# Performance work log

Measured on AMD Instinct MI355X. Metric: run time of the kernel, lower is better.

The kernel has to match this reference:

```python
import jax, jax.numpy as jnp
import numpy as np

N_BUS, N_LINE, N_GEN, N_LOAD = 1000, 2000, 100, 500
MAXSTEPS = 10  # matches ACOPF.maxsteps default
RIDGE = 1e-6  # tiny Tikhonov term for a robust normal-equation solve


def setup_inputs() -> dict:
    rng = np.random.default_rng(0)
    perm = rng.permutation(N_BUS)
    gen_buses = np.sort(perm[:N_GEN]).astype(np.int32)
    load_buses = np.sort(perm[N_GEN:N_GEN + N_LOAD]).astype(np.int32)
    ref_bus_idx = int(gen_buses[0])  # slack bus is a generator bus
    nongen_idx = np.setdiff1d(np.arange(N_BUS), gen_buses).astype(np.int32)
    nonref_idx = np.delete(np.arange(N_BUS), ref_bus_idx).astype(np.int32)
    line_from = rng.integers(0, N_BUS, N_LINE).astype(np.int32)
    line_to = ((line_from + rng.integers(1, N_BUS, N_LINE)) % N_BUS).astype(np.int32)

    ks = jax.random.split(jax.random.key(0), 12)
    u = lambda k, n, lo, hi: jax.random.uniform(k, (n,), jnp.float32, lo, hi)
    line_g = u(ks[0], N_LINE, 1.0, 5.0)
    line_b = -u(ks[1], N_LINE, 5.0, 15.0)
    shunt_g = u(ks[2], N_BUS, 0.0, 0.05)
    shunt_b = u(ks[3], N_BUS, 0.0, 0.05)
    tap = 1.0 + u(ks[4], N_LINE, -0.05, 0.05)
    shift = u(ks[5], N_LINE, -0.05, 0.05)
    charging = u(ks[6], N_LINE, 0.0, 0.05)
    P_gen = u(ks[7], N_GEN, 0.0, 0.5)
    V_gen = jnp.ones((N_GEN,), jnp.float32)
    P_load = u(ks[8], N_LOAD, 0.0, 0.1)
    Q_load = u(ks[9], N_LOAD, 0.0, 0.05)
    bus_v_limits = jnp.stack(
        [jnp.full((N_BUS,), 0.94, jnp.float32), jnp.full((N_BUS,), 1.06, jnp.float32)], axis=1)

    return dict(
        line_g=line_g, line_b=line_b, shunt_g=shunt_g, shunt_b=shunt_b,
        tap=tap, shift=shift, charging=charging,
        P_gen=P_gen, V_gen=V_gen, P_load=P_load, Q_load=Q_load,
        bus_v_limits=bus_v_limits,
        line_from=jnp.asarray(line_from), line_to=jnp.asarray(line_to),
        gen_buses=jnp.asarray(gen_buses), load_buses=jnp.asarray(load_buses),
        nongen_idx=jnp.asarray(nongen_idx), nonref_idx=jnp.asarray(nonref_idx),
        ref_bus_idx=ref_bus_idx,
    )


def _admittance_coo(line_from, line_to, line_g, line_b, shunt_g, shunt_b, tap, shift, charging, n_bus):
    # Standard pi-model branch admittances with transformer taps/phase shifts.
    ys = line_g.astype(jnp.complex64) + 1j * line_b.astype(jnp.complex64)
    bc = 1j * (charging.astype(jnp.complex64) / 2)
    tc = tap.astype(jnp.complex64) * jnp.exp(1j * shift.astype(jnp.complex64))
    Yff = (ys + bc) / (tap * tap)
    Ytt = ys + bc
    Yft = -ys / jnp.conj(tc)
    Ytf = -ys / tc
    diag = jnp.arange(n_bus, dtype=line_from.dtype)
    rows = jnp.concatenate([line_from, line_to, line_from, line_to, diag])
    cols = jnp.concatenate([line_from, line_to, line_to, line_from, diag])
    vals = jnp.concatenate([Yff, Ytt, Yft, Ytf,
                            shunt_g.astype(jnp.complex64) + 1j * shunt_b.astype(jnp.complex64)])
    return rows, cols, vals


def reference(line_g, line_b, shunt_g, shunt_b, tap, shift, charging,
              P_gen, V_gen, P_load, Q_load, bus_v_limits,
              line_from, line_to, gen_buses, load_buses,
              nongen_idx, nonref_idx, ref_bus_idx):
    n_bus = shunt_g.shape[0]
    n_nongen = nongen_idx.shape[0]
    rows, cols, vals = _admittance_coo(line_from, line_to, line_g, line_b,
                                       shunt_g, shunt_b, tap, shift, charging, n_bus)

    def injections(Vm, Va):
        V = Vm * jnp.exp(1j * Va)  # [n_bus] complex64
        current = jax.ops.segment_sum(vals * V[cols], rows, num_segments=n_bus)  # sparse Y @ V
        S = V * jnp.conj(current)
        return S.real, S.imag

    def residual(x):
        Vm = jnp.zeros(n_bus, jnp.float32).at[gen_buses].set(V_gen).at[nongen_idx].set(x[:n_nongen])
        Va = jnp.zeros(n_bus, jnp.float32).at[nonref_idx].set(x[n_nongen:])
        P, Q = injections(Vm, Va)
        P = P.at[gen_buses].add(-P_gen).at[load_buses].add(-P_load)
        Q = Q.at[load_buses].add(-Q_load)
        return jnp.concatenate([P[nonref_idx], Q[nongen_idx]])

    @jax.checkpoint
    def gn_step(x):
        r = residual(x)
        J = jax.jacfwd(residual)(x)  # [n_res, n_x]
        JtJ = J.T @ J + RIDGE * jnp.eye(J.shape[1], dtype=J.dtype)
        dx = jnp.linalg.solve(JtJ, J.T @ r)
        return x - dx

    x = jnp.concatenate([jnp.ones(n_nongen, jnp.float32),
                         jnp.zeros(n_bus - 1, jnp.float32)])
    for _ in range(MAXSTEPS):
        x = gn_step(x)

    r_final = residual(x)
    acopf_residual = (r_final ** 2).sum()

    Vm = jnp.zeros(n_bus, jnp.float32).at[gen_buses].set(V_gen).at[nongen_idx].set(x[:n_nongen])
    Va = jnp.zeros(n_bus, jnp.float32).at[nonref_idx].set(x[n_nongen:])

    # complete_powers
    P, Q = injections(Vm, Va)
    P = P.at[gen_buses].add(-P_gen).at[load_buses].add(-P_load)
    Q = Q.at[load_buses].add(-Q_load)
    Q_gen = Q[gen_buses]
    P_ref = P[ref_bus_idx]
    Q_ref = Q[ref_bus_idx]

    # voltage constraint violations
    V_min, V_max = bus_v_limits[:, 0], bus_v_limits[:, 1]
    V_violation = jax.nn.relu(Vm - V_max) + jax.nn.relu(V_min - Vm)

    return Vm, Va, Q_gen, P_ref, Q_ref, acopf_residual, V_violation
```

## Files before the change

### kernel.cpp

```cpp
#include <hip/hip_runtime.h>
#include <hip/hip_bf16.h>


#define NBUS 1000
#define NLINE 2000
#define NE   (2*NLINE)
#define NGEN 100
#define NLOAD 500
#define NTH 1024
#define NWAVE (NTH/64)
#define MAXSTEPS 10
#define KCG_MAX 600
#define RIDGE_F 1e-6f
#define TOL_REL 1e-10

struct Ws {
  int   vm_pos[NBUS];
  int   va_pos[NBUS];
  float Pspec[NBUS];
  float Qspec[NBUS];
  float Vgb[NBUS];
  int   rank_f[NLINE];
  int   rank_t[NLINE];
};

__device__ __forceinline__ float rdf(const void* p, int i, int bf) {
  if (bf) {
    unsigned int u = ((unsigned int)(((const unsigned short*)p)[i])) << 16;
    return __uint_as_float(u);
  }
  return ((const float*)p)[i];
}
__device__ __forceinline__ void wrf(void* p, int i, float v, int bf) {
  if (bf) {
    unsigned int u = __float_as_uint(v);
    unsigned int r = (u + 0x7fffu + ((u >> 16) & 1u)) >> 16;
    ((unsigned short*)p)[i] = (unsigned short)r;
  } else {
    ((float*)p)[i] = v;
  }
}
__device__ __forceinline__ int detect_bf(const void* p) {
  const unsigned short* h = (const unsigned short*)p;
  int ok = 1;
#pragma unroll
  for (int i = 0; i < 8; ++i) {
    float v = __uint_as_float(((unsigned int)h[i]) << 16);
    ok &= (v > 0.25f && v < 8.0f) ? 1 : 0;
  }
  return ok;
}
__device__ __forceinline__ int lbound(const int* a, int n, int v) {
  int lo = 0, hi = n;
  while (lo < hi) { int m = (lo + hi) >> 1; if (a[m] < v) lo = m + 1; else hi = m; }
  return lo;
}

struct In {
  const void *lg, *lb, *tp, *sh, *ch;
  const int *lf, *lt;
  int bf;
};
struct LineY { int f, t; float ffr, ffi, ttr, tti, ftr, fti, tfr, tfi; };

__device__ __forceinline__ LineY line_y(const In& I, int l) {
  LineY L;
  double g = rdf(I.lg, l, I.bf), b = rdf(I.lb, l, I.bf);
  double t = rdf(I.tp, l, I.bf), s = rdf(I.sh, l, I.bf);
  double c = rdf(I.ch, l, I.bf) * 0.5;
  double sn, cs;
  sincos(s, &sn, &cs);
  double it = 1.0 / t, it2 = it * it;
  L.f = I.lf[l]; L.t = I.lt[l];
  L.ffr = (float)(g * it2);                 L.ffi = (float)((b + c) * it2);
  L.ttr = (float)g;                         L.tti = (float)(b + c);
  L.ftr = (float)(-(g * cs - b * sn) * it); L.fti = (float)(-(g * sn + b * cs) * it);
  L.tfr = (float)(-(g * cs + b * sn) * it); L.tfi = (float)(-(b * cs - g * sn) * it);
  return L;
}

__device__ __forceinline__ float blk_sumf(float v, float* red) {
#pragma unroll
  for (int o = 32; o > 0; o >>= 1) v += __shfl_down(v, o, 64);
  if ((threadIdx.x & 63) == 0) red[threadIdx.x >> 6] = v;
  __syncthreads();
  const float4* r4 = (const float4*)red;
  float s = 0.f;
#pragma unroll
  for (int w = 0; w < NWAVE / 4; ++w) {
    float4 t = r4[w];
    s += t.x; s += t.y; s += t.z; s += t.w;
  }
  return s;
}

__global__ void setup_k(const void* lg, const void* Pg, const void* Vg,
                        const void* Pl, const void* Ql,
                        const int* gen_b, const int* load_b, const int* refp,
                        const int* lf, const int* lt,
                        Ws* __restrict__ W) {
  __shared__ int slf[NLINE], slt[NLINE];
  int bf = detect_bf(lg);
  int t = blockIdx.x * blockDim.x + threadIdx.x;
  for (int i = threadIdx.x; i < NLINE; i += blockDim.x) { slf[i] = lf[i]; slt[i] = lt[i]; }
  __syncthreads();
  int ref = refp[0];
  if (t < NBUS) {
    int gl = lbound(gen_b, NGEN, t);
    int isg = (gl < NGEN && gen_b[gl] == t) ? 1 : 0;
    int ll = lbound(load_b, NLOAD, t);
    int isl = (ll < NLOAD && load_b[ll] == t) ? 1 : 0;
    W->vm_pos[t] = isg ? -1 : (t - gl);
    W->va_pos[t] = (t == ref) ? -1 : (t - ((t > ref) ? 1 : 0));
    float ps = 0.f, qs = 0.f;
    if (isg) ps += rdf(Pg, gl, bf);
    if (isl) { ps += rdf(Pl, ll, bf); qs += rdf(Ql, ll, bf); }
    W->Pspec[t] = ps;
    W->Qspec[t] = qs;
    W->Vgb[t] = isg ? rdf(Vg, gl, bf) : 1.0f;
  }
  if (t < NLINE) {
    int f = slf[t], tt = slt[t], rf = 0, rt = 0;
    for (int l = 0; l < t; ++l) {
      int a = slf[l], b = slt[l];
      rf += (a == f) + (b == f);
      rt += (a == tt) + (b == tt);
    }
    W->rank_f[t] = rf;
    W->rank_t[t] = rt;
  }
}

__global__ void __launch_bounds__(NTH)
solver_k(const void* lg, const void* lb, const void* shg, const void* shb,
         const void* tp, const void* sh, const void* ch, const void* limits,
         const int* lf, const int* lt, const int* gen_b, const int* refp,
         const Ws* __restrict__ W, void* __restrict__ out) {
  __shared__ int rs_[NBUS + 1];
  __shared__ unsigned short cidx_[NE];
  __shared__ float2 fwd_[NE];
  __shared__ float2 rev_[NE];
  __shared__ float2 ev_[NE];
  __shared__ float2 stp_[NBUS];
  __shared__ float2 sts_[NBUS];
  __shared__ float2 ab_[NBUS];
  __shared__ float2 mk_[NBUS];
  __shared__ __align__(16) float red_[2][NWAVE];

  const int tid = threadIdx.x;
  const bool own = (tid < NBUS);
  In I;
  I.lg = lg; I.lb = lb; I.tp = tp; I.sh = sh; I.ch = ch;
  I.lf = lf; I.lt = lt;
  I.bf = detect_bf(lg);
  const int bf = I.bf;

  int* scanA = (int*)ev_;
  int* scanB = ((int*)ev_) + NTH;

  int vp = -1, ap = -1;
  float mng = 0.f, mnr = 0.f, Pspec = 0.f, Qspec = 0.f, Vgb = 1.f;
  if (own) {
    vp = W->vm_pos[tid]; ap = W->va_pos[tid];
    mng = (vp >= 0) ? 1.f : 0.f;
    mnr = (ap >= 0) ? 1.f : 0.f;
    Pspec = W->Pspec[tid]; Qspec = W->Qspec[tid]; Vgb = W->Vgb[tid];
    mk_[tid] = make_float2(mnr, mng);
  }
  scanA[tid] = 0;
  __syncthreads();
  for (int l = tid; l < NLINE; l += NTH) {
    atomicAdd(&scanA[lf[l]], 1);
    atomicAdd(&scanA[lt[l]], 1);
  }
  __syncthreads();
  {
    int* src = scanA; int* dst = scanB;
    for (int off = 1; off < NTH; off <<= 1) {
      int v = src[tid] + ((tid >= off) ? src[tid - off] : 0);
      dst[tid] = v;
      __syncthreads();
      int* t = src; src = dst; dst = t;
    }
    if (tid == 0) rs_[0] = 0;
    if (own) rs_[tid + 1] = src[tid];
  }
  __syncthreads();
  for (int l = tid; l < NLINE; l += NTH) {
    LineY L = line_y(I, l);
    int pf = rs_[L.f] + W->rank_f[l];
    int pt = rs_[L.t] + W->rank_t[l];
    cidx_[pf] = (unsigned short)L.t;
    fwd_[pf] = make_float2(L.ftr, L.fti);
    rev_[pf] = make_float2(L.tfr, L.tfi);
    ev_[pf]  = make_float2(L.ffr, L.ffi);
    cidx_[pt] = (unsigned short)L.f;
    fwd_[pt] = make_float2(L.tfr, L.tfi);
    rev_[pt] = make_float2(L.ftr, L.fti);
    ev_[pt]  = make_float2(L.ttr, L.tti);
  }
  __syncthreads();
  float Gkk = 0.f, Bkk = 0.f;
  int rs0 = 0, rs1 = 0;
  if (own) {
    rs0 = rs_[tid]; rs1 = rs_[tid + 1];
    double G = rdf(shg, tid, bf), B = rdf(shb, tid, bf);
    for (int e = rs0; e < rs1; ++e) { float2 d = ev_[e]; G += d.x; B += d.y; }
    Gkk = (float)G; Bkk = (float)B;
  }
  __syncthreads();

  #define EDGE_JVP_S(SRC) \
    for (int k = 0; k < 4; ++k) { \
      int e = tid + k * NTH; \
      if (e < NE) { \
        int j = cidx_[e]; float2 f = fwd_[e], v = SRC[j]; \
        ev_[e] = make_float2(f.x * v.x - f.y * v.y, f.x * v.y + f.y * v.x); \
      } \
    }
  #define EDGE_VJP(SRC) \
    for (int k = 0; k < 4; ++k) { \
      int e = tid + k * NTH; \
      if (e < NE) { \
        int j = cidx_[e]; float2 r = rev_[e], w = SRC[j]; \
        ev_[e] = make_float2(r.x * w.x + r.y * w.y, r.x * w.y - r.y * w.x); \
      } \
    }

  double xvm = 1.0, xva = 0.0;
  int par = 0;
  double gabs = 0.0;

  for (int outer = 0; outer < MAXSTEPS; ++outer) {
    float av = 0.f, bv = 0.f, ca = 1.f, sa = 0.f;
    if (own) {
      double Vm = (vp >= 0) ? xvm : (double)Vgb;
      double Va = (ap >= 0) ? xva : 0.0;
      double snd, csd;
      sincos(Va, &snd, &csd);
      ca = (float)csd; sa = (float)snd;
      av = (float)(Vm * csd); bv = (float)(Vm * snd);
      ab_[tid] = make_float2(av, bv);
    }
    __syncthreads();
    EDGE_JVP_S(ab_)
    __syncthreads();
    float cI = 0.f, dI = 0.f, wPp = 0.f, wQq = 0.f;
    float M11 = 0.f, M12 = 0.f, M22 = 0.f;
    if (own) {
      double cId = (double)Gkk * av - (double)Bkk * bv;
      double dId = (double)Gkk * bv + (double)Bkk * av;
      for (int e = rs0; e < rs1; ++e) { float2 v = ev_[e]; cId += v.x; dId += v.y; }
      cI = (float)cId; dI = (float)dId;
      double P = (double)av * cId + (double)bv * dId - (double)Pspec;
      double Q = (double)bv * cId - (double)av * dId - (double)Qspec;
      wPp = (float)(mnr * P); wQq = (float)(mng * Q);
      sts_[tid] = make_float2(wPp * av + wQq * bv, wPp * bv - wQq * av);
      float w1r = ca * cI + sa * dI, w1i = sa * cI - ca * dI;
      float mr = Gkk * ca - Bkk * sa, mi = -(Gkk * sa + Bkk * ca);
      float ur0 = av * mr - bv * mi, ui0 = av * mi + bv * mr;
      float Tr = w1r + ur0, Ti = w1i + ui0;
      float w2r = av * dI - bv * cI, w2i = av * cI + bv * dI;
      float wr0 = Gkk * av - Bkk * bv, wi0 = Gkk * bv + Bkk * av;
      float zr0 = av * wr0 + bv * wi0, zi0 = bv * wr0 - av * wi0;
      float Uor = w2r + zi0, Uoi = w2i - zr0;
      float Avv = mnr * Tr * Tr + mng * Ti * Ti;
      float Aaa = mnr * Uor * Uor + mng * Uoi * Uoi;
      float Ava = mnr * Tr * Uor + mng * Ti * Uoi;
      for (int e = rs0; e < rs1; ++e) {
        int j = cidx_[e]; float2 r = rev_[e], vj = ab_[j], mj = mk_[j];
        float mrr = r.x * ca - r.y * sa, mii = -(r.x * sa + r.y * ca);
        float ur = vj.x * mrr - vj.y * mii, ui = vj.x * mii + vj.y * mrr;
        float wr = r.x * av - r.y * bv, wi = r.x * bv + r.y * av;
        float zr = vj.x * wr + vj.y * wi, zi = vj.y * wr - vj.x * wi;
        Avv += mj.x * ur * ur + mj.y * ui * ui;
        Aaa += mj.x * zi * zi + mj.y * zr * zr;
        Ava += mj.x * ur * zi - mj.y * ui * zr;
      }
      float A11 = Avv + RIDGE_F, A22 = Aaa + RIDGE_F;
      if (vp >= 0 && ap >= 0) {
        float id = 1.f / (A11 * A22 - Ava * Ava);
        M11 = A22 * id; M22 = A11 * id; M12 = -Ava * id;
      } else if (vp >= 0) M11 = 1.f / A11;
      else if (ap >= 0)  M22 = 1.f / A22;
    }
    __syncthreads();
    EDGE_VJP(sts_)
    __syncthreads();
    float g0vm = 0.f, g0va = 0.f;
    if (own) {
      float cb = wPp * av + wQq * bv, db2 = wPp * bv - wQq * av;
      double sda = (double)wPp * cI - (double)wQq * dI + (double)Gkk * cb + (double)Bkk * db2;
      double sdb = (double)wPp * dI + (double)wQq * cI - (double)Bkk * cb + (double)Gkk * db2;
      for (int e = rs0; e < rs1; ++e) { float2 v = ev_[e]; sda += v.x; sdb += v.y; }
      g0vm = (float)(mng * (ca * sda + sa * sdb));
      g0va = (float)(mnr * (-bv * sda + av * sdb));
    }
    float rvm = g0vm, rva = g0va, dxvm = 0.f, dxva = 0.f;
    float zvm = M11 * rvm + M12 * rva, zva = M12 * rvm + M22 * rva;
    float pvm = zvm, pva = zva;
    float tzx = 0.f, tzy = 0.f, tpx = 0.f, tpy = 0.f;
    if (own) {
      tzx = zvm * ca - zva * bv; tzy = zvm * sa + zva * av;
      tpx = tzx; tpy = tzy;
      stp_[tid] = make_float2(tpx, tpy);
    }
    float part = own ? (rvm * zvm + rva * zva) : 0.f;
    double gamma = (double)blk_sumf(part, red_[par]); par ^= 1;
    const double gamma0 = gamma;
    if (outer == 0) gabs = 0.1 * TOL_REL * gamma0;
    const double thr = fmax(gamma0 * TOL_REL, gabs);

    if (gamma0 > thr) {
      for (int it = 0; it < KCG_MAX; ++it) {
        EDGE_JVP_S(stp_)
        __syncthreads();
        float qP = 0.f, qQ = 0.f;
        float dpart = 0.f;
        if (own) {
          float dc = Gkk * tpx - Bkk * tpy, dd = Gkk * tpy + Bkk * tpx;
          for (int e = rs0; e < rs1; ++e) { float2 v = ev_[e]; dc += v.x; dd += v.y; }
          float dP = tpx * cI + av * dc + tpy * dI + bv * dd;
          float dQ = tpy * cI + bv * dc - tpx * dI - av * dd;
          qP = mnr * dP; qQ = mng * dQ;
          sts_[tid] = make_float2(qP * av + qQ * bv, qP * bv - qQ * av);
          dpart = qP * dP + qQ * dQ + RIDGE_F * (pvm * pvm + pva * pva);
        }
        double delta = (double)blk_sumf(dpart, red_[par]); par ^= 1;
        if (!(delta > 0.0)) break;
        float af = (float)(gamma / delta);
        EDGE_VJP(sts_)
        __syncthreads();
        if (own) {
          dxvm += af * pvm; dxva += af * pva;
          float cb = qP * av + qQ * bv, db2 = qP * bv - qQ * av;
          float sda = qP * cI - qQ * dI + Gkk * cb + Bkk * db2;
          float sdb = qP * dI + qQ * cI - Bkk * cb + Gkk * db2;
          for (int e = rs0; e < rs1; ++e) { float2 v = ev_[e]; sda += v.x; sdb += v.y; }
          float yvm = mng * (ca * sda + sa * sdb);
          float yva = mnr * (-bv * sda + av * sdb);
          rvm -= af * (yvm + RIDGE_F * pvm);
          rva -= af * (yva + RIDGE_F * pva);
        }
        if ((it & 63) == 63) {
          float tda = 0.f, tdb = 0.f;
          if (own) {
            tda = dxvm * ca - dxva * bv;
            tdb = dxvm * sa + dxva * av;
            sts_[tid] = make_float2(tda, tdb);
          }
          __syncthreads();
          EDGE_JVP_S(sts_)
          __syncthreads();
          float rqP = 0.f, rqQ = 0.f;
          if (own) {
            float dc = Gkk * tda - Bkk * tdb, dd = Gkk * tdb + Bkk * tda;
            for (int e = rs0; e < rs1; ++e) { float2 v = ev_[e]; dc += v.x; dd += v.y; }
            float dP = tda * cI + av * dc + tdb * dI + bv * dd;
            float dQ = tdb * cI + bv * dc - tda * dI - av * dd;
            rqP = mnr * dP; rqQ = mng * dQ;
            sts_[tid] = make_float2(rqP * av + rqQ * bv, rqP * bv - rqQ * av);
          }
          __syncthreads();
          EDGE_VJP(sts_)
          __syncthreads();
          if (own) {
            float cb = rqP * av + rqQ * bv, db2 = rqP * bv - rqQ * av;
            float sda = rqP * cI - rqQ * dI + Gkk * cb + Bkk * db2;
            float sdb = rqP * dI + rqQ * cI - Bkk * cb + Gkk * db2;
            for (int e = rs0; e < rs1; ++e) { float2 v = ev_[e]; sda += v.x; sdb += v.y; }
            float tvm = mng * (ca * sda + sa * sdb);
            float tva = mnr * (-bv * sda + av * sdb);
            rvm = g0vm - tvm - RIDGE_F * dxvm;
            rva = g0va - tva - RIDGE_F * dxva;
          }
        }
        float gpart = 0.f;
        if (own) {
          zvm = M11 * rvm + M12 * rva; zva = M12 * rvm + M22 * rva;
          tzx = zvm * ca - zva * bv; tzy = zvm * sa + zva * av;
          gpart = rvm * zvm + rva * zva;
        }
        double gamma2 = (double)blk_sumf(gpart, red_[par]); par ^= 1;
        if (gamma2 <= thr || !(gamma2 > 0.0)) break;
        float bt = (float)(gamma2 / gamma);
        gamma = gamma2;
        if (own) {
          pvm = zvm + bt * pvm; pva = zva + bt * pva;
          tpx = tzx + bt * tpx; tpy = tzy + bt * tpy;
          stp_[tid] = make_float2(tpx, tpy);
        }
        __syncthreads();
      }
    }
    if (own) { xvm -= (double)dxvm; xva -= (double)dxva; }
    __syncthreads();
  }

  float Vmf = 1.f, Vaf = 0.f, av = 0.f, bv = 0.f;
  if (own) {
    double Vm = (vp >= 0) ? xvm : (double)Vgb;
    double Va = (ap >= 0) ? xva : 0.0;
    double snd, csd;
    sincos(Va, &snd, &csd);
    Vmf = (float)Vm; Vaf = (float)Va;
    av = (float)(Vm * csd); bv = (float)(Vm * snd);
    ab_[tid] = make_float2(av, bv);
  }
  __syncthreads();
  EDGE_JVP_S(ab_)
  __syncthreads();
  float P = 0.f, Q = 0.f;
  if (own) {
    double cId = (double)Gkk * av - (double)Bkk * bv;
    double dId = (double)Gkk * bv + (double)Bkk * av;
    for (int e = rs0; e < rs1; ++e) { float2 v = ev_[e]; cId += v.x; dId += v.y; }
    P = (float)((double)av * cId + (double)bv * dId - (double)Pspec);
    Q = (float)((double)bv * cId - (double)av * dId - (double)Qspec);
    sts_[tid] = make_float2(P, Q);
  }
  __syncthreads();
  float rpart = own ? (mnr * P * P + mng * Q * Q) : 0.f;
  float rsum = blk_sumf(rpart, red_[par]); par ^= 1;
  if (own) {
    wrf(out, tid, Vmf, bf);
    wrf(out, NBUS + tid, Vaf, bf);
    float vmin = rdf(limits, 2 * tid, bf), vmax = rdf(limits, 2 * tid + 1, bf);
    float viol = fmaxf(Vmf - vmax, 0.f) + fmaxf(vmin - Vmf, 0.f);
    wrf(out, 2103 + tid, viol, bf);
  }
  if (tid < NGEN) wrf(out, 2000 + tid, sts_[gen_b[tid]].y, bf);
  if (tid == 0) {
    int ref = refp[0];
    wrf(out, 2100, sts_[ref].x, bf);
    wrf(out, 2101, sts_[ref].y, bf);
    wrf(out, 2102, rsum, bf);
  }
}

extern "C" void kernel_launch(void* const* d_in, const int* in_sizes, int n_in,
                              void* d_out, int out_size, void* d_ws, size_t ws_size,
                              hipStream_t stream) {
  const void* line_g   = d_in[0];
  const void* line_b   = d_in[1];
  const void* shunt_g  = d_in[2];
  const void* shunt_b  = d_in[3];
  const void* tap      = d_in[4];
  const void* shift    = d_in[5];
  const void* charging = d_in[6];
  const void* P_gen    = d_in[7];
  const void* V_gen    = d_in[8];
  const void* P_load   = d_in[9];
  const void* Q_load   = d_in[10];
  const void* limits   = d_in[11];
  const int* line_from = (const int*)d_in[12];
  const int* line_to   = (const int*)d_in[13];
  const int* gen_b     = (const int*)d_in[14];
  const int* load_b    = (const int*)d_in[15];
  const int* refp      = (const int*)d_in[18];

  if (ws_size < sizeof(Ws)) return;
  Ws* W = (Ws*)d_ws;

  setup_k<<<dim3(8), dim3(256), 0, stream>>>(line_g, P_gen, V_gen, P_load, Q_load,
                                             gen_b, load_b, refp,
                                             line_from, line_to, W);
  solver_k<<<dim3(1), dim3(NTH), 0, stream>>>(line_g, line_b, shunt_g, shunt_b,
                                              tap, shift, charging, limits,
                                              line_from, line_to, gen_b, refp,
                                              W, d_out);
}
```

Baseline: 1.908 ms.

## Assign edges per wavefront to drop block barriers after edge products

```diff
diff --git a/kernel.cpp b/kernel.cpp
--- a/kernel.cpp
+++ b/kernel.cpp
@@ -140,7 +140,7 @@
   __shared__ unsigned short cidx_[NE];
   __shared__ float2 fwd_[NE];
   __shared__ float2 rev_[NE];
-  __shared__ float2 ev_[NE];
+  __shared__ float2 ev_[NE + NBUS];
   __shared__ float2 stp_[NBUS];
   __shared__ float2 sts_[NBUS];
   __shared__ float2 ab_[NBUS];
@@ -210,22 +210,43 @@
   }
   __syncthreads();
 
-  #define EDGE_JVP_S(SRC) \
-    for (int k = 0; k < 4; ++k) { \
-      int e = tid + k * NTH; \
-      if (e < NE) { \
-        int j = cidx_[e]; float2 f = fwd_[e], v = SRC[j]; \
-        ev_[e] = make_float2(f.x * v.x - f.y * v.y, f.x * v.y + f.y * v.x); \
+  const int prs0 = rs0 + tid, prs1 = rs1 + tid;
+
+  const int wv = tid >> 6, ln = tid & 63;
+  const int wb0 = wv * 64;
+  const int wb1 = (wb0 + 64 < NBUS) ? wb0 + 64 : NBUS;
+  const int ws0 = rs_[wb0], ws1 = rs_[wb1];
+  int   sj[8]; float2 sf[8], sr[8]; int sp[8]; bool sv[8];
+#pragma unroll
+  for (int k = 0; k < 8; ++k) {
+    int s = ws0 + ln + 64 * k;
+    bool v = (s < ws1);
+    sv[k] = v;
+    int ss = v ? s : ws0;
+    sj[k] = cidx_[ss]; sf[k] = fwd_[ss]; sr[k] = rev_[ss];
+    int lo = wb0, hi = wb1;
+    while (lo + 1 < hi) { int m = (lo + hi) >> 1; if (rs_[m] <= ss) lo = m; else hi = m; }
+    sp[k] = ss + lo;
+  }
+
+  #define WJVP(SRC) \
+    _Pragma("unroll") \
+    for (int k = 0; k < 8; ++k) { \
+      if (sv[k]) { \
+        int j = sj[k]; float2 f = sf[k], v = SRC[j]; \
+        ev_[sp[k]] = make_float2(f.x * v.x - f.y * v.y, f.x * v.y + f.y * v.x); \
       } \
-    }
-  #define EDGE_VJP(SRC) \
-    for (int k = 0; k < 4; ++k) { \
-      int e = tid + k * NTH; \
-      if (e < NE) { \
-        int j = cidx_[e]; float2 r = rev_[e], w = SRC[j]; \
-        ev_[e] = make_float2(r.x * w.x + r.y * w.y, r.x * w.y - r.y * w.x); \
+    } \
+    asm volatile("" ::: "memory");
+  #define WVJP(SRC) \
+    _Pragma("unroll") \
+    for (int k = 0; k < 8; ++k) { \
+      if (sv[k]) { \
+        int j = sj[k]; float2 r = sr[k], w = SRC[j]; \
+        ev_[sp[k]] = make_float2(r.x * w.x + r.y * w.y, r.x * w.y - r.y * w.x); \
       } \
-    }
+    } \
+    asm volatile("" ::: "memory");
 
   double xvm = 1.0, xva = 0.0;
   int par = 0;
@@ -243,14 +264,13 @@
       ab_[tid] = make_float2(av, bv);
     }
     __syncthreads();
-    EDGE_JVP_S(ab_)
-    __syncthreads();
+    WJVP(ab_)
     float cI = 0.f, dI = 0.f, wPp = 0.f, wQq = 0.f;
     float M11 = 0.f, M12 = 0.f, M22 = 0.f;
     if (own) {
       double cId = (double)Gkk * av - (double)Bkk * bv;
       double dId = (double)Gkk * bv + (double)Bkk * av;
-      for (int e = rs0; e < rs1; ++e) { float2 v = ev_[e]; cId += v.x; dId += v.y; }
+      for (int e = prs0; e < prs1; ++e) { float2 v = ev_[e]; cId += v.x; dId += v.y; }
       cI = (float)cId; dI = (float)dId;
       double P = (double)av * cId + (double)bv * dId - (double)Pspec;
       double Q = (double)bv * cId - (double)av * dId - (double)Qspec;
@@ -285,14 +305,13 @@
       else if (ap >= 0)  M22 = 1.f / A22;
     }
     __syncthreads();
-    EDGE_VJP(sts_)
-    __syncthreads();
+    WVJP(sts_)
     float g0vm = 0.f, g0va = 0.f;
     if (own) {
       float cb = wPp * av + wQq * bv, db2 = wPp * bv - wQq * av;
       double sda = (double)wPp * cI - (double)wQq * dI + (double)Gkk * cb + (double)Bkk * db2;
       double sdb = (double)wPp * dI + (double)wQq * cI - (double)Bkk * cb + (double)Gkk * db2;
-      for (int e = rs0; e < rs1; ++e) { float2 v = ev_[e]; sda += v.x; sdb += v.y; }
+      for (int e = prs0; e < prs1; ++e) { float2 v = ev_[e]; sda += v.x; sdb += v.y; }
       g0vm = (float)(mng * (ca * sda + sa * sdb));
       g0va = (float)(mnr * (-bv * sda + av * sdb));
     }
@@ -313,13 +332,12 @@
 
     if (gamma0 > thr) {
       for (int it = 0; it < KCG_MAX; ++it) {
-        EDGE_JVP_S(stp_)
-        __syncthreads();
+        WJVP(stp_)
         float qP = 0.f, qQ = 0.f;
         float dpart = 0.f;
         if (own) {
           float dc = Gkk * tpx - Bkk * tpy, dd = Gkk * tpy + Bkk * tpx;
-          for (int e = rs0; e < rs1; ++e) { float2 v = ev_[e]; dc += v.x; dd += v.y; }
+          for (int e = prs0; e < prs1; ++e) { float2 v = ev_[e]; dc += v.x; dd += v.y; }
           float dP = tpx * cI + av * dc + tpy * dI + bv * dd;
           float dQ = tpy * cI + bv * dc - tpx * dI - av * dd;
           qP = mnr * dP; qQ = mng * dQ;
@@ -329,20 +347,20 @@
         double delta = (double)blk_sumf(dpart, red_[par]); par ^= 1;
         if (!(delta > 0.0)) break;
         float af = (float)(gamma / delta);
-        EDGE_VJP(sts_)
-        __syncthreads();
+        WVJP(sts_)
         if (own) {
           dxvm += af * pvm; dxva += af * pva;
           float cb = qP * av + qQ * bv, db2 = qP * bv - qQ * av;
           float sda = qP * cI - qQ * dI + Gkk * cb + Bkk * db2;
           float sdb = qP * dI + qQ * cI - Bkk * cb + Gkk * db2;
-          for (int e = rs0; e < rs1; ++e) { float2 v = ev_[e]; sda += v.x; sdb += v.y; }
+          for (int e = prs0; e < prs1; ++e) { float2 v = ev_[e]; sda += v.x; sdb += v.y; }
           float yvm = mng * (ca * sda + sa * sdb);
           float yva = mnr * (-bv * sda + av * sdb);
           rvm -= af * (yvm + RIDGE_F * pvm);
           rva -= af * (yva + RIDGE_F * pva);
         }
         if ((it & 63) == 63) {
+          __syncthreads();
           float tda = 0.f, tdb = 0.f;
           if (own) {
             tda = dxvm * ca - dxva * bv;
@@ -350,25 +368,24 @@
             sts_[tid] = make_float2(tda, tdb);
           }
           __syncthreads();
-          EDGE_JVP_S(sts_)
-          __syncthreads();
+          WJVP(sts_)
           float rqP = 0.f, rqQ = 0.f;
           if (own) {
             float dc = Gkk * tda - Bkk * tdb, dd = Gkk * tdb + Bkk * tda;
-            for (int e = rs0; e < rs1; ++e) { float2 v = ev_[e]; dc += v.x; dd += v.y; }
+            for (int e = prs0; e < prs1; ++e) { float2 v = ev_[e]; dc += v.x; dd += v.y; }
             float dP = tda * cI + av * dc + tdb * dI + bv * dd;
             float dQ = tdb * cI + bv * dc - tda * dI - av * dd;
             rqP = mnr * dP; rqQ = mng * dQ;
-            sts_[tid] = make_float2(rqP * av + rqQ * bv, rqP * bv - rqQ * av);
           }
           __syncthreads();
-          EDGE_VJP(sts_)
+          if (own) sts_[tid] = make_float2(rqP * av + rqQ * bv, rqP * bv - rqQ * av);
           __syncthreads();
+          WVJP(sts_)
           if (own) {
             float cb = rqP * av + rqQ * bv, db2 = rqP * bv - rqQ * av;
             float sda = rqP * cI - rqQ * dI + Gkk * cb + Bkk * db2;
             float sdb = rqP * dI + rqQ * cI - Bkk * cb + Gkk * db2;
-            for (int e = rs0; e < rs1; ++e) { float2 v = ev_[e]; sda += v.x; sdb += v.y; }
+            for (int e = prs0; e < prs1; ++e) { float2 v = ev_[e]; sda += v.x; sdb += v.y; }
             float tvm = mng * (ca * sda + sa * sdb);
             float tva = mnr * (-bv * sda + av * sdb);
             rvm = g0vm - tvm - RIDGE_F * dxvm;
@@ -408,13 +425,12 @@
     ab_[tid] = make_float2(av, bv);
   }
   __syncthreads();
-  EDGE_JVP_S(ab_)
-  __syncthreads();
+  WJVP(ab_)
   float P = 0.f, Q = 0.f;
   if (own) {
     double cId = (double)Gkk * av - (double)Bkk * bv;
     double dId = (double)Gkk * bv + (double)Bkk * av;
-    for (int e = rs0; e < rs1; ++e) { float2 v = ev_[e]; cId += v.x; dId += v.y; }
+    for (int e = prs0; e < prs1; ++e) { float2 v = ev_[e]; cId += v.x; dId += v.y; }
     P = (float)((double)av * cId + (double)bv * dId - (double)Pspec);
     Q = (float)((double)bv * cId - (double)av * dId - (double)Qspec);
     sts_[tid] = make_float2(P, Q);
```

Result: slower. 2.393 ms (+25.4%).
